# Kernel optimization log

Measured on AMD Instinct MI355X. Metric: run time of the kernel, lower is better.

## Reference

```python
import jax, jax.numpy as jnp
import numpy as np

TEMPERATURE = 0.07
LOSS_CL_WEIGHT = 1.0
EPS = 1e-12  # F.normalize default eps


def setup_inputs() -> dict:
    key = jax.random.key(0)
    k1, k2 = jax.random.split(key)
    N, S, D = 64, 64, 256
    return {
        "proj_z1": jax.random.normal(k1, (N, S, D), dtype=jnp.float32),
        "proj_z2": jax.random.normal(k2, (N, S, D), dtype=jnp.float32),
    }


def _clean_normalize(x, NS, D):
    # flatten -> replace nan/inf with 0 -> L2 normalize rows
    x = x.reshape(NS, D)
    x = jnp.where(jnp.isfinite(x), x, jnp.zeros((), x.dtype))
    norm = jnp.linalg.norm(x, axis=1, keepdims=True)
    return x / jnp.maximum(norm, EPS)


def reference(proj_z1, proj_z2):
    N, S, D = proj_z1.shape
    NS = N * S
    M = 2 * NS
    f1 = _clean_normalize(proj_z1, NS, D)
    f2 = _clean_normalize(proj_z2, NS, D)
    features = jnp.concatenate([f1, f2], axis=0)          # (M, D)
    sim = features @ features.T                            # (M, M)

    idx = jnp.arange(M)
    # positive pair: row i <-> row (i + NS) mod M (eye blocks in label_matrix)
    positives = sim[idx, (idx + NS) % M] / TEMPERATURE     # (M,)
    # CE denominator = all off-diagonal entries (positives + negatives)
    scores = sim / TEMPERATURE
    scores = jnp.where(idx[:, None] == idx[None, :], -jnp.inf, scores)
    lse = jax.nn.logsumexp(scores, axis=1)                 # (M,)
    loss = jnp.mean(lse - positives)
    return LOSS_CL_WEIGHT * loss
```

## Files before the change

### kernel.cpp

```cpp
#include <hip/hip_runtime.h>
#include <hip/hip_bf16.h>
#include <stdint.h>

#define NS_ 4096
#define M_  8192
#define D_  256
#define TEMP 0.07f
#define EXP_SCALE 20.61707212818536f
#define LN2 0.6931471805599453f

typedef short bf16x8 __attribute__((ext_vector_type(8)));
typedef float f32x4  __attribute__((ext_vector_type(4)));
typedef unsigned short ushortx4 __attribute__((ext_vector_type(4)));

static __device__ inline unsigned short f2bf(float x) {
    unsigned u = __float_as_uint(x);
    u += 0x7fffu + ((u >> 16) & 1u);
    return (unsigned short)(u >> 16);
}

static __device__ inline float cleanf(float v) {
    return __builtin_isfinite(v) ? v : 0.0f;
}

#define LDS_LOAD16(gp, lp) \
    __builtin_amdgcn_global_load_lds((const __attribute__((address_space(1))) uint32_t*)(gp), \
                                     (__attribute__((address_space(3))) uint32_t*)(lp), 16, 0, 0)

__global__ __launch_bounds__(64) void knorm(const float* __restrict__ z1,
                                            const float* __restrict__ z2,
                                            short* __restrict__ F,
                                            float* __restrict__ pos,
                                            float* __restrict__ denom,
                                            int* __restrict__ cnt,
                                            float* __restrict__ out) {
    const int i = blockIdx.x;
    const int t = threadIdx.x;
    const float4* p1 = (const float4*)(z1 + (size_t)i * D_);
    const float4* p2 = (const float4*)(z2 + (size_t)i * D_);
    float4 a = p1[t], b = p2[t];
    a.x = cleanf(a.x); a.y = cleanf(a.y); a.z = cleanf(a.z); a.w = cleanf(a.w);
    b.x = cleanf(b.x); b.y = cleanf(b.y); b.z = cleanf(b.z); b.w = cleanf(b.w);

    float s1 = a.x*a.x + a.y*a.y + a.z*a.z + a.w*a.w;
    float s2 = b.x*b.x + b.y*b.y + b.z*b.z + b.w*b.w;
    float dp = a.x*b.x + a.y*b.y + a.z*b.z + a.w*b.w;
    #pragma unroll
    for (int m = 1; m < 64; m <<= 1) {
        s1 += __shfl_xor(s1, m);
        s2 += __shfl_xor(s2, m);
        dp += __shfl_xor(dp, m);
    }
    const float inv1 = 1.0f / fmaxf(sqrtf(s1), 1e-12f);
    const float inv2 = 1.0f / fmaxf(sqrtf(s2), 1e-12f);

    ushortx4 o1, o2;
    o1.x = f2bf(a.x * inv1); o1.y = f2bf(a.y * inv1); o1.z = f2bf(a.z * inv1); o1.w = f2bf(a.w * inv1);
    o2.x = f2bf(b.x * inv2); o2.y = f2bf(b.y * inv2); o2.z = f2bf(b.z * inv2); o2.w = f2bf(b.w * inv2);
    ((ushortx4*)(F + (size_t)i * D_))[t]          = o1;
    ((ushortx4*)(F + (size_t)(i + NS_) * D_))[t]  = o2;

    if (t == 0) pos[i] = dp * inv1 * inv2;
    if (t < 2)  denom[i * 2 + t] = 0.0f;
    if (i == 0 && t < 32) cnt[t] = 0;
    if (i == 0 && t == 0) out[0] = 0.0f;
}

__global__ __launch_bounds__(256, 2) void kgemm(const short* __restrict__ F,
                                                float* __restrict__ denom,
                                                int* __restrict__ cnt,
                                                const float* __restrict__ pos,
                                                float* __restrict__ out) {
    __shared__ short Bl[64 * 256];
    __shared__ int lastflag;
    __shared__ float red[4];

    const int rtile = blockIdx.x >> 4;
    const int cq    = blockIdx.x & 15;
    const int R0 = rtile * 256;
    const int C0 = cq * 512;

    const int tid  = threadIdx.x;
    const int lane = tid & 63;
    const int wave = tid >> 6;
    const int c16  = lane & 15;
    const int quad = lane >> 4;
    const int swz  = c16 & 7;

    int goff[8];
    #pragma unroll
    for (int r2 = 0; r2 < 8; ++r2) {
        int c    = tid + r2 * 256;
        int row  = c >> 5;
        int kg   = (c & 31) ^ (row & 7);
        goff[r2] = row * D_ + kg * 8;
    }

    bf16x8 afrag[4][8];
    const int arow_l = wave * 16 + c16;
    #pragma unroll
    for (int ch = 0; ch < 4; ++ch) {
        __syncthreads();
        const short* ga = F + (size_t)(R0 + ch * 64) * D_;
        #pragma unroll
        for (int r2 = 0; r2 < 8; ++r2)
            LDS_LOAD16(ga + goff[r2], Bl + (tid + r2 * 256) * 8);
        __syncthreads();
        #pragma unroll
        for (int ks = 0; ks < 8; ++ks)
            afrag[ch][ks] = *(const bf16x8*)(Bl + arow_l * 256 +
                                             (((ks * 4 + quad) ^ (arow_l & 7)) * 8));
    }

    float accexp[4][4];
    #pragma unroll
    for (int s = 0; s < 4; ++s)
        #pragma unroll
        for (int r = 0; r < 4; ++r) accexp[s][r] = 0.0f;

    for (int it = 0; it < 8; ++it) {
        __syncthreads();
        const short* gb = F + (size_t)(C0 + it * 64) * D_;
        #pragma unroll
        for (int r2 = 0; r2 < 8; ++r2)
            LDS_LOAD16(gb + goff[r2], Bl + (tid + r2 * 256) * 8);
        __syncthreads();

        #pragma unroll
        for (int sub = 0; sub < 4; ++sub) {
            const int tc = sub * 16 + c16;
            bf16x8 bfrag[8];
            #pragma unroll
            for (int ks = 0; ks < 8; ++ks)
                bfrag[ks] = *(const bf16x8*)(Bl + tc * 256 +
                                             (((ks * 4 + quad) ^ swz) * 8));
            f32x4 acc[4];
            #pragma unroll
            for (int s = 0; s < 4; ++s) acc[s] = (f32x4){0.f, 0.f, 0.f, 0.f};
            #pragma unroll
            for (int ks = 0; ks < 8; ++ks)
                #pragma unroll
                for (int s = 0; s < 4; ++s)
                    acc[s] = __builtin_amdgcn_mfma_f32_16x16x32_bf16(
                        afrag[s][ks], bfrag[ks], acc[s], 0, 0, 0);

            const int colbase = C0 + it * 64 + sub * 16;
            #pragma unroll
            for (int s = 0; s < 4; ++s) {
                const int rowbase = R0 + s * 64 + wave * 16;
                if (colbase != rowbase) {
                    #pragma unroll
                    for (int r = 0; r < 4; ++r)
                        accexp[s][r] += __builtin_amdgcn_exp2f(acc[s][r] * EXP_SCALE);
                } else {
                    #pragma unroll
                    for (int r = 0; r < 4; ++r) {
                        float e = __builtin_amdgcn_exp2f(acc[s][r] * EXP_SCALE);
                        if (c16 == quad * 4 + r) e = 0.0f;
                        accexp[s][r] += e;
                    }
                }
            }
        }
    }

    #pragma unroll
    for (int s = 0; s < 4; ++s)
        #pragma unroll
        for (int r = 0; r < 4; ++r) {
            float v = accexp[s][r];
            v += __shfl_xor(v, 1);
            v += __shfl_xor(v, 2);
            v += __shfl_xor(v, 4);
            v += __shfl_xor(v, 8);
            if (c16 == 0)
                atomicAdd(&denom[R0 + s * 64 + wave * 16 + quad * 4 + r], v);
        }

    __syncthreads();
    if (tid == 0) {
        __threadfence();
        lastflag = (atomicAdd(&cnt[rtile], 1) == 15);
    }
    __syncthreads();
    if (lastflag) {
        __threadfence();
        float v = atomicAdd(&denom[R0 + tid], 0.0f);
        float p = __builtin_amdgcn_logf(v) * (LN2 / (float)M_);
        #pragma unroll
        for (int m = 1; m < 64; m <<= 1) p += __shfl_xor(p, m);
        if (lane == 0) red[wave] = p;
        __syncthreads();
        if (tid == 0) atomicAdd(out, red[0] + red[1] + red[2] + red[3]);
        if (rtile == 0) {
            __syncthreads();
            float sp = 0.0f;
            for (int i = tid; i < NS_; i += 256) sp += pos[i];
            #pragma unroll
            for (int m = 1; m < 64; m <<= 1) sp += __shfl_xor(sp, m);
            if (lane == 0) red[wave] = sp;
            __syncthreads();
            if (tid == 0)
                atomicAdd(out, (red[0] + red[1] + red[2] + red[3]) *
                               (-2.0f / (TEMP * (float)M_)));
        }
    }
}

extern "C" void kernel_launch(void* const* d_in, const int* in_sizes, int n_in,
                              void* d_out, int out_size, void* d_ws, size_t ws_size,
                              hipStream_t stream) {
    const float* z1 = (const float*)d_in[0];
    const float* z2 = (const float*)d_in[1];

    short* F     = (short*)d_ws;
    float* denom = (float*)((char*)d_ws + (size_t)M_ * D_ * 2);
    int*   cnt   = (int*)(denom + M_);
    float* pos   = (float*)(cnt + 32);
    float* out   = (float*)d_out;

    knorm<<<NS_, 64, 0, stream>>>(z1, z2, F, pos, denom, cnt, out);
    kgemm<<<512, 256, 0, stream>>>(F, denom, cnt, pos, out);
}
```

Baseline: 109.1 us.

## Halve GEMM row tile to 128 and raise occupancy to four blocks per CU

The row tile per block shrinks from 256 to 128, doubling the grid to 1024 blocks, and the launch bound moves to 4 blocks per CU. Each wave now holds 2 instead of 4 A fragments, which lowers register pressure and allows more waves to hide LDS and exp latency. The trade-off is that each B tile load from LDS and global memory feeds half as many MFMAs, doubling total B traffic. The completion counter array grows to 64 entries to match.

```diff
diff --git a/kernel.cpp b/kernel.cpp
--- a/kernel.cpp
+++ b/kernel.cpp
@@ -8,6 +8,7 @@
 #define TEMP 0.07f
 #define EXP_SCALE 20.61707212818536f
 #define LN2 0.6931471805599453f
+#define CQ_ 16
 
 typedef short bf16x8 __attribute__((ext_vector_type(8)));
 typedef float f32x4  __attribute__((ext_vector_type(4)));
@@ -62,11 +63,11 @@
 
     if (t == 0) pos[i] = dp * inv1 * inv2;
     if (t < 2)  denom[i * 2 + t] = 0.0f;
-    if (i == 0 && t < 32) cnt[t] = 0;
+    if (i == 0) cnt[t] = 0;
     if (i == 0 && t == 0) out[0] = 0.0f;
 }
 
-__global__ __launch_bounds__(256, 2) void kgemm(const short* __restrict__ F,
+__global__ __launch_bounds__(256, 4) void kgemm(const short* __restrict__ F,
                                                 float* __restrict__ denom,
                                                 int* __restrict__ cnt,
                                                 const float* __restrict__ pos,
@@ -77,7 +78,7 @@
 
     const int rtile = blockIdx.x >> 4;
     const int cq    = blockIdx.x & 15;
-    const int R0 = rtile * 256;
+    const int R0 = rtile * 128;
     const int C0 = cq * 512;
 
     const int tid  = threadIdx.x;
@@ -87,34 +88,34 @@
     const int quad = lane >> 4;
     const int swz  = c16 & 7;
 
-    int goff[8];
-    #pragma unroll
-    for (int r2 = 0; r2 < 8; ++r2) {
-        int c    = tid + r2 * 256;
-        int row  = c >> 5;
-        int kg   = (c & 31) ^ (row & 7);
-        goff[r2] = row * D_ + kg * 8;
-    }
-
-    bf16x8 afrag[4][8];
-    const int arow_l = wave * 16 + c16;
-    #pragma unroll
-    for (int ch = 0; ch < 4; ++ch) {
+    bf16x8 afrag[2][8];
+    #pragma unroll
+    for (int ch = 0; ch < 2; ++ch) {
         __syncthreads();
         const short* ga = F + (size_t)(R0 + ch * 64) * D_;
         #pragma unroll
-        for (int r2 = 0; r2 < 8; ++r2)
-            LDS_LOAD16(ga + goff[r2], Bl + (tid + r2 * 256) * 8);
-        __syncthreads();
-        #pragma unroll
-        for (int ks = 0; ks < 8; ++ks)
-            afrag[ch][ks] = *(const bf16x8*)(Bl + arow_l * 256 +
-                                             (((ks * 4 + quad) ^ (arow_l & 7)) * 8));
-    }
-
-    float accexp[4][4];
-    #pragma unroll
-    for (int s = 0; s < 4; ++s)
+        for (int r2 = 0; r2 < 8; ++r2) {
+            int c   = tid + r2 * 256;
+            int row = c >> 5;
+            int kg  = (c & 31) ^ (row & 7);
+            LDS_LOAD16(ga + row * D_ + kg * 8, Bl + c * 8);
+        }
+        __syncthreads();
+        if ((wave >> 1) == ch) {
+            #pragma unroll
+            for (int s = 0; s < 2; ++s) {
+                const int lr = (wave & 1) * 32 + s * 16 + c16;
+                #pragma unroll
+                for (int ks = 0; ks < 8; ++ks)
+                    afrag[s][ks] = *(const bf16x8*)(Bl + lr * 256 +
+                                                    (((ks * 4 + quad) ^ (lr & 7)) * 8));
+            }
+        }
+    }
+
+    float accexp[2][4];
+    #pragma unroll
+    for (int s = 0; s < 2; ++s)
         #pragma unroll
         for (int r = 0; r < 4; ++r) accexp[s][r] = 0.0f;
 
@@ -122,40 +123,49 @@
         __syncthreads();
         const short* gb = F + (size_t)(C0 + it * 64) * D_;
         #pragma unroll
-        for (int r2 = 0; r2 < 8; ++r2)
-            LDS_LOAD16(gb + goff[r2], Bl + (tid + r2 * 256) * 8);
+        for (int r2 = 0; r2 < 8; ++r2) {
+            int c   = tid + r2 * 256;
+            int row = c >> 5;
+            int kg  = (c & 31) ^ (row & 7);
+            LDS_LOAD16(gb + row * D_ + kg * 8, Bl + c * 8);
+        }
         __syncthreads();
 
         #pragma unroll
         for (int sub = 0; sub < 4; ++sub) {
             const int tc = sub * 16 + c16;
-            bf16x8 bfrag[8];
-            #pragma unroll
-            for (int ks = 0; ks < 8; ++ks)
-                bfrag[ks] = *(const bf16x8*)(Bl + tc * 256 +
-                                             (((ks * 4 + quad) ^ swz) * 8));
-            f32x4 acc[4];
-            #pragma unroll
-            for (int s = 0; s < 4; ++s) acc[s] = (f32x4){0.f, 0.f, 0.f, 0.f};
-            #pragma unroll
-            for (int ks = 0; ks < 8; ++ks)
+            const short* bbase = Bl + tc * 256;
+            f32x4 acc0 = (f32x4){0.f, 0.f, 0.f, 0.f};
+            f32x4 acc1 = (f32x4){0.f, 0.f, 0.f, 0.f};
+            #pragma unroll
+            for (int h = 0; h < 2; ++h) {
+                bf16x8 bfrag[4];
                 #pragma unroll
-                for (int s = 0; s < 4; ++s)
-                    acc[s] = __builtin_amdgcn_mfma_f32_16x16x32_bf16(
-                        afrag[s][ks], bfrag[ks], acc[s], 0, 0, 0);
+                for (int k2 = 0; k2 < 4; ++k2)
+                    bfrag[k2] = *(const bf16x8*)(bbase +
+                                 ((((h * 4 + k2) * 4 + quad) ^ swz) * 8));
+                #pragma unroll
+                for (int k2 = 0; k2 < 4; ++k2) {
+                    acc0 = __builtin_amdgcn_mfma_f32_16x16x32_bf16(
+                        afrag[0][h * 4 + k2], bfrag[k2], acc0, 0, 0, 0);
+                    acc1 = __builtin_amdgcn_mfma_f32_16x16x32_bf16(
+                        afrag[1][h * 4 + k2], bfrag[k2], acc1, 0, 0, 0);
+                }
+            }
 
             const int colbase = C0 + it * 64 + sub * 16;
             #pragma unroll
-            for (int s = 0; s < 4; ++s) {
-                const int rowbase = R0 + s * 64 + wave * 16;
+            for (int s = 0; s < 2; ++s) {
+                const f32x4 acc = s ? acc1 : acc0;
+                const int rowbase = R0 + wave * 32 + s * 16;
                 if (colbase != rowbase) {
                     #pragma unroll
                     for (int r = 0; r < 4; ++r)
-                        accexp[s][r] += __builtin_amdgcn_exp2f(acc[s][r] * EXP_SCALE);
+                        accexp[s][r] += __builtin_amdgcn_exp2f(acc[r] * EXP_SCALE);
                 } else {
                     #pragma unroll
                     for (int r = 0; r < 4; ++r) {
-                        float e = __builtin_amdgcn_exp2f(acc[s][r] * EXP_SCALE);
+                        float e = __builtin_amdgcn_exp2f(acc[r] * EXP_SCALE);
                         if (c16 == quad * 4 + r) e = 0.0f;
                         accexp[s][r] += e;
                     }
@@ -165,7 +175,7 @@
     }
 
     #pragma unroll
-    for (int s = 0; s < 4; ++s)
+    for (int s = 0; s < 2; ++s)
         #pragma unroll
         for (int r = 0; r < 4; ++r) {
             float v = accexp[s][r];
@@ -174,19 +184,22 @@
             v += __shfl_xor(v, 4);
             v += __shfl_xor(v, 8);
             if (c16 == 0)
-                atomicAdd(&denom[R0 + s * 64 + wave * 16 + quad * 4 + r], v);
+                atomicAdd(&denom[R0 + wave * 32 + s * 16 + quad * 4 + r], v);
         }
 
     __syncthreads();
     if (tid == 0) {
         __threadfence();
-        lastflag = (atomicAdd(&cnt[rtile], 1) == 15);
+        lastflag = (atomicAdd(&cnt[rtile], 1) == CQ_ - 1);
     }
     __syncthreads();
     if (lastflag) {
-        __threadfence();
-        float v = atomicAdd(&denom[R0 + tid], 0.0f);
-        float p = __builtin_amdgcn_logf(v) * (LN2 / (float)M_);
+        float p = 0.0f;
+        if (tid < 128) {
+            __threadfence();
+            float v = atomicAdd(&denom[R0 + tid], 0.0f);
+            p = __builtin_amdgcn_logf(v) * (LN2 / (float)M_);
+        }
         #pragma unroll
         for (int m = 1; m < 64; m <<= 1) p += __shfl_xor(p, m);
         if (lane == 0) red[wave] = p;
@@ -216,9 +229,9 @@
     short* F     = (short*)d_ws;
     float* denom = (float*)((char*)d_ws + (size_t)M_ * D_ * 2);
     int*   cnt   = (int*)(denom + M_);
-    float* pos   = (float*)(cnt + 32);
+    float* pos   = (float*)(cnt + 64);
     float* out   = (float*)d_out;
 
     knorm<<<NS_, 64, 0, stream>>>(z1, z2, F, pos, denom, cnt, out);
-    kgemm<<<512, 256, 0, stream>>>(F, denom, cnt, pos, out);
-}
+    kgemm<<<64 * CQ_, 256, 0, stream>>>(F, denom, cnt, pos, out);
+}
```

Result: slower. 138.5 us (+27.0%).

## Give each wave private double-buffered LDS staging and drop block barriers in GEMM

Applied to the files above, without the earlier changes.

The GEMM kernel now gives each wave its own LDS region. Each wave loads its own 64 A rows and streams 16-column B tiles through a private double buffer, using vmcnt waits in place of block-wide __syncthreads, so global loads overlap the MFMA and exp work. In exchange, each wave fetches the full B stream itself, which raises the redundant global and L2 traffic fourfold. The norm kernel now packs four rows per 256-thread block, and the zeroing of denom and cnt is rewritten to use global thread indices.

```diff
diff --git a/kernel.cpp b/kernel.cpp
--- a/kernel.cpp
+++ b/kernel.cpp
@@ -8,6 +8,7 @@
 #define TEMP 0.07f
 #define EXP_SCALE 20.61707212818536f
 #define LN2 0.6931471805599453f
+#define CQ_ 16
 
 typedef short bf16x8 __attribute__((ext_vector_type(8)));
 typedef float f32x4  __attribute__((ext_vector_type(4)));
@@ -27,15 +28,16 @@
     __builtin_amdgcn_global_load_lds((const __attribute__((address_space(1))) uint32_t*)(gp), \
                                      (__attribute__((address_space(3))) uint32_t*)(lp), 16, 0, 0)
 
-__global__ __launch_bounds__(64) void knorm(const float* __restrict__ z1,
-                                            const float* __restrict__ z2,
-                                            short* __restrict__ F,
-                                            float* __restrict__ pos,
-                                            float* __restrict__ denom,
-                                            int* __restrict__ cnt,
-                                            float* __restrict__ out) {
-    const int i = blockIdx.x;
-    const int t = threadIdx.x;
+__global__ __launch_bounds__(256) void knorm(const float* __restrict__ z1,
+                                             const float* __restrict__ z2,
+                                             short* __restrict__ F,
+                                             float* __restrict__ pos,
+                                             float* __restrict__ denom,
+                                             int* __restrict__ cnt,
+                                             float* __restrict__ out) {
+    const int wave = threadIdx.x >> 6;
+    const int t    = threadIdx.x & 63;
+    const int i    = blockIdx.x * 4 + wave;
     const float4* p1 = (const float4*)(z1 + (size_t)i * D_);
     const float4* p2 = (const float4*)(z2 + (size_t)i * D_);
     float4 a = p1[t], b = p2[t];
@@ -61,9 +63,10 @@
     ((ushortx4*)(F + (size_t)(i + NS_) * D_))[t]  = o2;
 
     if (t == 0) pos[i] = dp * inv1 * inv2;
-    if (t < 2)  denom[i * 2 + t] = 0.0f;
-    if (i == 0 && t < 32) cnt[t] = 0;
-    if (i == 0 && t == 0) out[0] = 0.0f;
+    const int gid = blockIdx.x * 256 + threadIdx.x;
+    if (gid < M_)  denom[gid] = 0.0f;
+    if (gid < 64)  cnt[gid] = 0;
+    if (gid == 0)  out[0] = 0.0f;
 }
 
 __global__ __launch_bounds__(256, 2) void kgemm(const short* __restrict__ F,
@@ -71,7 +74,7 @@
                                                 int* __restrict__ cnt,
                                                 const float* __restrict__ pos,
                                                 float* __restrict__ out) {
-    __shared__ short Bl[64 * 256];
+    __shared__ short Bl[4][8192];
     __shared__ int lastflag;
     __shared__ float red[4];
 
@@ -87,82 +90,92 @@
     const int quad = lane >> 4;
     const int swz  = c16 & 7;
 
-    int goff[8];
-    #pragma unroll
-    for (int r2 = 0; r2 < 8; ++r2) {
-        int c    = tid + r2 * 256;
-        int row  = c >> 5;
-        int kg   = (c & 31) ^ (row & 7);
-        goff[r2] = row * D_ + kg * 8;
-    }
+    short* myb = &Bl[wave][0];
 
     bf16x8 afrag[4][8];
-    const int arow_l = wave * 16 + c16;
-    #pragma unroll
-    for (int ch = 0; ch < 4; ++ch) {
-        __syncthreads();
-        const short* ga = F + (size_t)(R0 + ch * 64) * D_;
-        #pragma unroll
-        for (int r2 = 0; r2 < 8; ++r2)
-            LDS_LOAD16(ga + goff[r2], Bl + (tid + r2 * 256) * 8);
-        __syncthreads();
-        #pragma unroll
-        for (int ks = 0; ks < 8; ++ks)
-            afrag[ch][ks] = *(const bf16x8*)(Bl + arow_l * 256 +
-                                             (((ks * 4 + quad) ^ (arow_l & 7)) * 8));
-    }
-
-    float accexp[4][4];
-    #pragma unroll
-    for (int s = 0; s < 4; ++s)
-        #pragma unroll
-        for (int r = 0; r < 4; ++r) accexp[s][r] = 0.0f;
-
-    for (int it = 0; it < 8; ++it) {
-        __syncthreads();
-        const short* gb = F + (size_t)(C0 + it * 64) * D_;
-        #pragma unroll
-        for (int r2 = 0; r2 < 8; ++r2)
-            LDS_LOAD16(gb + goff[r2], Bl + (tid + r2 * 256) * 8);
-        __syncthreads();
-
-        #pragma unroll
-        for (int sub = 0; sub < 4; ++sub) {
-            const int tc = sub * 16 + c16;
-            bf16x8 bfrag[8];
+    #pragma unroll
+    for (int h = 0; h < 2; ++h) {
+        const short* ga = F + (size_t)(R0 + wave * 64 + h * 32) * D_;
+        #pragma unroll
+        for (int i = 0; i < 16; ++i) {
+            int c   = i * 64 + lane;
+            int row = c >> 5;
+            int kg  = (c & 31) ^ (row & 7);
+            LDS_LOAD16(ga + row * D_ + kg * 8, myb + c * 8);
+        }
+        asm volatile("s_waitcnt vmcnt(0)" ::: "memory");
+        #pragma unroll
+        for (int s2 = 0; s2 < 2; ++s2) {
+            const int lr = s2 * 16 + c16;
             #pragma unroll
             for (int ks = 0; ks < 8; ++ks)
-                bfrag[ks] = *(const bf16x8*)(Bl + tc * 256 +
-                                             (((ks * 4 + quad) ^ swz) * 8));
-            f32x4 acc[4];
+                afrag[h * 2 + s2][ks] = *(const bf16x8*)(myb + lr * 256 +
+                                         (((ks * 4 + quad) ^ swz) * 8));
+        }
+        asm volatile("s_waitcnt lgkmcnt(0)" ::: "memory");
+    }
+
+    float accexp[4][4];
+    #pragma unroll
+    for (int s = 0; s < 4; ++s)
+        #pragma unroll
+        for (int r = 0; r < 4; ++r) accexp[s][r] = 0.0f;
+
+    #define STAGE(t) do {                                                   \
+        const short* _gb = F + (size_t)(C0 + (t) * 16) * D_;                \
+        short* _dst = myb + ((t) & 1) * 4096;                               \
+        _Pragma("unroll")                                                   \
+        for (int _i = 0; _i < 8; ++_i) {                                    \
+            int _c   = _i * 64 + lane;                                      \
+            int _row = _c >> 5;                                             \
+            int _kg  = (_c & 31) ^ (_row & 7);                              \
+            LDS_LOAD16(_gb + _row * D_ + _kg * 8, _dst + _c * 8);           \
+        }                                                                   \
+    } while (0)
+
+    STAGE(0);
+    STAGE(1);
+    for (int t = 0; t < 32; ++t) {
+        if (t < 31) asm volatile("s_waitcnt vmcnt(8)" ::: "memory");
+        else        asm volatile("s_waitcnt vmcnt(0)" ::: "memory");
+
+        const short* bb = myb + (t & 1) * 4096;
+        bf16x8 bfrag[8];
+        #pragma unroll
+        for (int ks = 0; ks < 8; ++ks)
+            bfrag[ks] = *(const bf16x8*)(bb + c16 * 256 +
+                                         (((ks * 4 + quad) ^ swz) * 8));
+        f32x4 acc[4];
+        #pragma unroll
+        for (int s = 0; s < 4; ++s) acc[s] = (f32x4){0.f, 0.f, 0.f, 0.f};
+        #pragma unroll
+        for (int ks = 0; ks < 8; ++ks)
             #pragma unroll
-            for (int s = 0; s < 4; ++s) acc[s] = (f32x4){0.f, 0.f, 0.f, 0.f};
-            #pragma unroll
-            for (int ks = 0; ks < 8; ++ks)
+            for (int s = 0; s < 4; ++s)
+                acc[s] = __builtin_amdgcn_mfma_f32_16x16x32_bf16(
+                    afrag[s][ks], bfrag[ks], acc[s], 0, 0, 0);
+
+        if (t + 2 < 32) STAGE(t + 2);
+
+        const int colbase = C0 + t * 16;
+        #pragma unroll
+        for (int s = 0; s < 4; ++s) {
+            const int rowbase = R0 + wave * 64 + s * 16;
+            if (colbase != rowbase) {
                 #pragma unroll
-                for (int s = 0; s < 4; ++s)
-                    acc[s] = __builtin_amdgcn_mfma_f32_16x16x32_bf16(
-                        afrag[s][ks], bfrag[ks], acc[s], 0, 0, 0);
-
-            const int colbase = C0 + it * 64 + sub * 16;
-            #pragma unroll
-            for (int s = 0; s < 4; ++s) {
-                const int rowbase = R0 + s * 64 + wave * 16;
-                if (colbase != rowbase) {
-                    #pragma unroll
-                    for (int r = 0; r < 4; ++r)
-                        accexp[s][r] += __builtin_amdgcn_exp2f(acc[s][r] * EXP_SCALE);
-                } else {
-                    #pragma unroll
-                    for (int r = 0; r < 4; ++r) {
-                        float e = __builtin_amdgcn_exp2f(acc[s][r] * EXP_SCALE);
-                        if (c16 == quad * 4 + r) e = 0.0f;
-                        accexp[s][r] += e;
-                    }
+                for (int r = 0; r < 4; ++r)
+                    accexp[s][r] += __builtin_amdgcn_exp2f(acc[s][r] * EXP_SCALE);
+            } else {
+                #pragma unroll
+                for (int r = 0; r < 4; ++r) {
+                    float e = __builtin_amdgcn_exp2f(acc[s][r] * EXP_SCALE);
+                    if (c16 == quad * 4 + r) e = 0.0f;
+                    accexp[s][r] += e;
                 }
             }
         }
     }
+    #undef STAGE
 
     #pragma unroll
     for (int s = 0; s < 4; ++s)
@@ -174,13 +187,13 @@
             v += __shfl_xor(v, 4);
             v += __shfl_xor(v, 8);
             if (c16 == 0)
-                atomicAdd(&denom[R0 + s * 64 + wave * 16 + quad * 4 + r], v);
+                atomicAdd(&denom[R0 + wave * 64 + s * 16 + quad * 4 + r], v);
         }
 
     __syncthreads();
     if (tid == 0) {
         __threadfence();
-        lastflag = (atomicAdd(&cnt[rtile], 1) == 15);
+        lastflag = (atomicAdd(&cnt[rtile], 1) == CQ_ - 1);
     }
     __syncthreads();
     if (lastflag) {
@@ -216,9 +229,9 @@
     short* F     = (short*)d_ws;
     float* denom = (float*)((char*)d_ws + (size_t)M_ * D_ * 2);
     int*   cnt   = (int*)(denom + M_);
-    float* pos   = (float*)(cnt + 32);
+    float* pos   = (float*)(cnt + 64);
     float* out   = (float*)d_out;
 
-    knorm<<<NS_, 64, 0, stream>>>(z1, z2, F, pos, denom, cnt, out);
-    kgemm<<<512, 256, 0, stream>>>(F, denom, cnt, pos, out);
-}
+    knorm<<<NS_ / 4, 256, 0, stream>>>(z1, z2, F, pos, denom, cnt, out);
+    kgemm<<<32 * CQ_, 256, 0, stream>>>(F, denom, cnt, pos, out);
+}
```

Result: slower. 111.6 us (+2.3%).
